# Kernel optimization log

Hardware: AMD Instinct MI355X
Metric: run time of the kernel (lower is better)

Reference implementation:

```python
import jax, jax.numpy as jnp
import numpy as np

HS = 1024
IMS = 4096
NHEAD = 16
EPS = 1e-5


def _layer_norm(x, g, b):
    mu = jnp.mean(x, axis=-1, keepdims=True)
    var = jnp.mean(jnp.square(x - mu), axis=-1, keepdims=True)
    return (x - mu) * jax.lax.rsqrt(var + EPS) * g + b


def setup_inputs() -> dict:
    key = jax.random.key(0)
    ks = jax.random.split(key, 10)
    B, S = 16, 512
    x = jax.random.normal(ks[0], (B, S, HS), dtype=jnp.float32)
    input_mask = jnp.zeros((B, S), dtype=jnp.float32)  # additive mask, 0 = attend
    sc = 0.02
    return {
        "x": x,
        "input_mask": input_mask,
        "qkv_w": jax.random.normal(ks[1], (3 * HS, HS), jnp.float32) * sc,
        "qkv_b": jnp.zeros((3 * HS,), jnp.float32),
        "attn_ow": jax.random.normal(ks[2], (HS, HS), jnp.float32) * sc,
        "attn_ob": jnp.zeros((HS,), jnp.float32),
        "ln1_g": jnp.ones((HS,), jnp.float32),
        "ln1_b": jnp.zeros((HS,), jnp.float32),
        "inter_w": jax.random.normal(ks[3], (IMS, HS), jnp.float32) * sc,
        "inter_b": jnp.zeros((IMS,), jnp.float32),
        "out_w": jax.random.normal(ks[4], (HS, IMS), jnp.float32) * sc,
        "out_b": jnp.zeros((HS,), jnp.float32),
        "ln2_g": jnp.ones((HS,), jnp.float32),
        "ln2_b": jnp.zeros((HS,), jnp.float32),
    }


def reference(x, input_mask, qkv_w, qkv_b, attn_ow, attn_ob, ln1_g, ln1_b,
              inter_w, inter_b, out_w, out_b, ln2_g, ln2_b):
    B, S, H = x.shape
    d = H // NHEAD
    # ---- self-attention block (pre_layer_norm=True, eval mode => no dropout) ----
    resid = x
    y = _layer_norm(x, ln1_g, ln1_b)
    qkv = jnp.einsum('bsh,eh->bse', y, qkv_w) + qkv_b  # [B,S,3H]
    q, k, v = jnp.split(qkv, 3, axis=-1)
    q = q.reshape(B, S, NHEAD, d)
    k = k.reshape(B, S, NHEAD, d)
    v = v.reshape(B, S, NHEAD, d)
    scores = jnp.einsum('bqnd,bknd->bnqk', q, k) / jnp.sqrt(jnp.float32(d))
    scores = scores + input_mask[:, None, None, :]  # additive padding mask
    probs = jax.nn.softmax(scores, axis=-1)
    ctx = jnp.einsum('bnqk,bknd->bqnd', probs, v).reshape(B, S, H)
    attn_out = jnp.einsum('bsh,oh->bso', ctx, attn_ow) + attn_ob
    x = resid + attn_out
    # ---- FFN block ----
    resid = x
    y = _layer_norm(x, ln2_g, ln2_b)
    h = jax.nn.relu(jnp.einsum('bsh,ih->bsi', y, inter_w) + inter_b)
    ffn_out = jnp.einsum('bsi,oi->bso', h, out_w) + out_b
    return resid + ffn_out
```

## Files before the change

### kernel.cpp

```cpp
#include <hip/hip_runtime.h>


using f32x4  = __attribute__((ext_vector_type(4))) float;
using f32x16 = __attribute__((ext_vector_type(16))) float;
using s16x8  = __attribute__((ext_vector_type(8))) short;
using i32x4  = __attribute__((ext_vector_type(4))) int;

__device__ __forceinline__ unsigned short f2bf(float f) {
    unsigned x = __builtin_bit_cast(unsigned, f);
    return (unsigned short)((x + 0x7fffu + ((x >> 16) & 1u)) >> 16);
}

#define GLL16(gptr, lptr)                                                     \
    __builtin_amdgcn_global_load_lds(                                         \
        (const __attribute__((address_space(1))) void*)(gptr),                \
        (__attribute__((address_space(3))) void*)(lptr), 16, 0, 0)

__global__ __launch_bounds__(256) void wconv_kernel(
    const float* __restrict__ w0, const float* __restrict__ w1,
    const float* __restrict__ w2, const float* __restrict__ w3,
    unsigned short* __restrict__ o0, unsigned short* __restrict__ o1,
    unsigned short* __restrict__ o2, unsigned short* __restrict__ o3) {
    long idx = (long)blockIdx.x * 256 + threadIdx.x;
    const float* src;
    unsigned short* dst;
    long rel;
    if (idx < 786432L)        { src = w0; dst = o0; rel = idx; }
    else if (idx < 1048576L)  { src = w1; dst = o1; rel = idx - 786432L; }
    else if (idx < 2097152L)  { src = w2; dst = o2; rel = idx - 1048576L; }
    else                      { src = w3; dst = o3; rel = idx - 2097152L; }
    float4 v = *(const float4*)(src + rel * 4);
    ushort4 o;
    o.x = f2bf(v.x); o.y = f2bf(v.y); o.z = f2bf(v.z); o.w = f2bf(v.w);
    *(ushort4*)(dst + rel * 4) = o;
}

__global__ __launch_bounds__(256) void ln_kernel(
    const float* __restrict__ x, const float* __restrict__ gw,
    const float* __restrict__ bw, unsigned short* __restrict__ y) {
    __shared__ float rbuf[8];
    const int row = blockIdx.x;
    const int t = threadIdx.x;
    const float* xr = x + (size_t)row * 1024;
    float4 v = *(const float4*)(xr + t * 4);
    float s  = v.x + v.y + v.z + v.w;
    float ss = v.x * v.x + v.y * v.y + v.z * v.z + v.w * v.w;
#pragma unroll
    for (int sh = 1; sh < 64; sh <<= 1) {
        s  += __shfl_xor(s, sh, 64);
        ss += __shfl_xor(ss, sh, 64);
    }
    int w = t >> 6;
    if ((t & 63) == 0) { rbuf[w * 2] = s; rbuf[w * 2 + 1] = ss; }
    __syncthreads();
    s  = rbuf[0] + rbuf[2] + rbuf[4] + rbuf[6];
    ss = rbuf[1] + rbuf[3] + rbuf[5] + rbuf[7];
    float mu  = s * (1.f / 1024.f);
    float var = ss * (1.f / 1024.f) - mu * mu;
    float rs  = rsqrtf(var + 1e-5f);
    float4 gv = *(const float4*)(gw + t * 4);
    float4 bv = *(const float4*)(bw + t * 4);
    ushort4 o;
    o.x = f2bf((v.x - mu) * rs * gv.x + bv.x);
    o.y = f2bf((v.y - mu) * rs * gv.y + bv.y);
    o.z = f2bf((v.z - mu) * rs * gv.z + bv.z);
    o.w = f2bf((v.w - mu) * rs * gv.w + bv.w);
    *(ushort4*)(y + (size_t)row * 1024 + t * 4) = o;
}

template <bool RELU, bool RESID, bool OUT_BF16>
__global__ __launch_bounds__(256, 2) void gemm_bt(
    const unsigned short* __restrict__ A, const unsigned short* __restrict__ Bw,
    const float* __restrict__ bias, const float* __restrict__ resid,
    void* __restrict__ Cout, int M, int N, int K) {
    __shared__ char smem[2 * 128 * 64 * 2];
    char* As = smem;
    char* Bs = smem + 128 * 64 * 2;

    const int tid = threadIdx.x;
    const int lane = tid & 63;
    const int w = tid >> 6;
    const int wr = w >> 1, wc = w & 1;
    const int g = lane >> 4;
    const int fr = lane & 15;
    const int m0 = blockIdx.y * 128;
    const int n0 = blockIdx.x * 128;

    f32x4 acc[4][4] = {};

    for (int kt = 0; kt < K; kt += 64) {
#pragma unroll
        for (int c = 0; c < 4; ++c) {
            int lin = (c * 256 + tid) * 16;
            int row = lin >> 7;
            int Lb = lin ^ ((row & 7) << 4);
            int colb = Lb & 127;
            const char* ga = (const char*)A + ((size_t)(m0 + row) * K + kt) * 2 + colb;
            const char* gb = (const char*)Bw + ((size_t)(n0 + row) * K + kt) * 2 + colb;
            GLL16(ga, As + lin);
            GLL16(gb, Bs + lin);
        }
        __syncthreads();
#pragma unroll
        for (int ks = 0; ks < 2; ++ks) {
            s16x8 af[4], bf[4];
#pragma unroll
            for (int mi = 0; mi < 4; ++mi) {
                int row = wr * 64 + mi * 16 + fr;
                int off = (row << 7) + ((ks * 64 + g * 16) ^ ((row & 7) << 4));
                af[mi] = *(const s16x8*)(As + off);
            }
#pragma unroll
            for (int ni = 0; ni < 4; ++ni) {
                int row = wc * 64 + ni * 16 + fr;
                int off = (row << 7) + ((ks * 64 + g * 16) ^ ((row & 7) << 4));
                bf[ni] = *(const s16x8*)(Bs + off);
            }
#pragma unroll
            for (int mi = 0; mi < 4; ++mi)
#pragma unroll
                for (int ni = 0; ni < 4; ++ni)
                    acc[mi][ni] = __builtin_amdgcn_mfma_f32_16x16x32_bf16(
                        af[mi], bf[ni], acc[mi][ni], 0, 0, 0);
        }
        __syncthreads();
    }

    float bv[4];
#pragma unroll
    for (int ni = 0; ni < 4; ++ni) bv[ni] = bias[n0 + wc * 64 + ni * 16 + fr];
#pragma unroll
    for (int mi = 0; mi < 4; ++mi) {
#pragma unroll
        for (int r = 0; r < 4; ++r) {
            int row = m0 + wr * 64 + mi * 16 + g * 4 + r;
#pragma unroll
            for (int ni = 0; ni < 4; ++ni) {
                int col = n0 + wc * 64 + ni * 16 + fr;
                float v = acc[mi][ni][r] + bv[ni];
                if (RELU) v = v > 0.f ? v : 0.f;
                if (RESID) v += resid[(size_t)row * N + col];
                if (OUT_BF16)
                    ((unsigned short*)Cout)[(size_t)row * N + col] = f2bf(v);
                else
                    ((float*)Cout)[(size_t)row * N + col] = v;
            }
        }
    }
}

__global__ __launch_bounds__(512, 2) void attn_kernel(
    const unsigned short* __restrict__ qkv, const float* __restrict__ mask,
    unsigned short* __restrict__ ctx) {
    extern __shared__ char smem[];

    const int tid = threadIdx.x;
    const int lane = tid & 63;
    const int w = tid >> 6;
    const int l31 = lane & 31;
    const int hi = lane >> 5;
    const int bh = blockIdx.x >> 1;
    const int b = bh >> 4, h = bh & 15;
    const int qt = (blockIdx.x & 1) * 256 + w * 32;

    const size_t rstr = 3072;
    const unsigned short* qbase = qkv + (size_t)b * 512 * rstr + h * 64;
    const unsigned short* kbase = qbase + 1024;
    const unsigned short* vbase = qbase + 2048;
    const float* mrow = mask + b * 512;

    s16x8 qf[4];
#pragma unroll
    for (int kc = 0; kc < 4; ++kc)
        qf[kc] = *(const s16x8*)(qbase + (size_t)(qt + l31) * rstr + kc * 16 + hi * 8);

    f32x16 O0 = {}, O1 = {};
    float m = -3e38f, l = 0.f;
    const int bpbase = 36 * hi * 4;

    auto stage = [&](int kt, int bufsel) {
        char* Kb = smem + bufsel * 16384;
        char* Vb = smem + 32768 + bufsel * 16384;
#pragma unroll
        for (int c = 0; c < 2; ++c) {
            int lin = (c * 512 + tid) * 16;
            int row = lin >> 7;
            int colb = (lin & 127) ^ ((row & 7) << 4);
            GLL16((const char*)kbase + (size_t)(kt * 128 + row) * rstr * 2 + colb,
                  Kb + lin);
        }
        int s = tid & 127, dg = tid >> 7;
        const unsigned short* vsrc = vbase + (size_t)(kt * 128 + s) * rstr + dg * 16;
        union { i32x4 v; unsigned short u[8]; } v0, v1;
        v0.v = *(const i32x4*)vsrc;
        v1.v = *(const i32x4*)(vsrc + 8);
#pragma unroll
        for (int j = 0; j < 8; ++j) {
            int d = dg * 16 + j;
            *(unsigned short*)(Vb + d * 256 + ((s * 2) ^ ((d & 15) << 4))) = v0.u[j];
        }
#pragma unroll
        for (int j = 0; j < 8; ++j) {
            int d = dg * 16 + 8 + j;
            *(unsigned short*)(Vb + d * 256 + ((s * 2) ^ ((d & 15) << 4))) = v1.u[j];
        }
    };

    const float C   = 0.18033688f;
    const float L2E = 1.44269504f;

    stage(0, 0);
    __syncthreads();

    for (int kt = 0; kt < 4; ++kt) {
        const int cur = kt & 1;
        if (kt < 3) stage(kt + 1, cur ^ 1);
        char* Kb = smem + cur * 16384;
        char* Vb = smem + 32768 + cur * 16384;
        const int swzk = (l31 & 7) << 4;

        f32x16 sc[4];
#pragma unroll
        for (int t = 0; t < 4; ++t) {
            f32x16 a = {};
#pragma unroll
            for (int kc = 0; kc < 4; ++kc) {
                s16x8 kf = *(const s16x8*)(Kb + (32 * t + l31) * 128 +
                                           ((kc * 32 + hi * 16) ^ swzk));
                a = __builtin_amdgcn_mfma_f32_32x32x16_bf16(kf, qf[kc], a, 0, 0, 0);
            }
            sc[t] = a;
        }

        float tm = -3e38f;
#pragma unroll
        for (int t = 0; t < 4; ++t) {
#pragma unroll
            for (int k2 = 0; k2 < 4; ++k2) {
                f32x4 mk = *(const f32x4*)(mrow + kt * 128 + 32 * t + 8 * k2 + 4 * hi);
#pragma unroll
                for (int i = 0; i < 4; ++i) {
                    float v = sc[t][4 * k2 + i] * C + mk[i] * L2E;
                    sc[t][4 * k2 + i] = v;
                    tm = fmaxf(tm, v);
                }
            }
        }
        tm = fmaxf(tm, __shfl_xor(tm, 32, 64));

        if (__any(tm > m + 11.0f)) {
            float mn = fmaxf(m, tm);
            float fac = exp2f(m - mn);
            m = mn;
            l *= fac;
            int fi = __float_as_int(fac);
#pragma unroll
            for (int r = 0; r < 16; ++r) {
                int q2 = (r & 3) + 8 * (r >> 2);
                float fq = __int_as_float(
                    __builtin_amdgcn_ds_bpermute(bpbase + q2 * 4, fi));
                O0[r] *= fq;
                O1[r] *= fq;
            }
        }

        float ts = 0.f;
#pragma unroll
        for (int t = 0; t < 4; ++t)
#pragma unroll
            for (int r = 0; r < 16; ++r) {
                float p = exp2f(sc[t][r] - m);
                sc[t][r] = p;
                ts += p;
            }
        ts += __shfl_xor(ts, 32, 64);
        l += ts;

        unsigned pk01[4][4], pk23[4][4];
#pragma unroll
        for (int t = 0; t < 4; ++t)
#pragma unroll
            for (int k = 0; k < 4; ++k) {
                unsigned r0, r1;
                asm("v_cvt_pk_bf16_f32 %0, %1, %2"
                    : "=v"(r0) : "v"(sc[t][4 * k]), "v"(sc[t][4 * k + 1]));
                asm("v_cvt_pk_bf16_f32 %0, %1, %2"
                    : "=v"(r1) : "v"(sc[t][4 * k + 2]), "v"(sc[t][4 * k + 3]));
                pk01[t][k] = r0;
                pk23[t][k] = r1;
            }

#pragma unroll
        for (int t = 0; t < 4; ++t)
#pragma unroll
            for (int cc = 0; cc < 2; ++cc) {
                unsigned a0 = pk01[t][2 * cc], b0 = pk01[t][2 * cc + 1];
                unsigned c0 = pk23[t][2 * cc], d0 = pk23[t][2 * cc + 1];
                asm("v_permlane32_swap_b32 %0, %1" : "+v"(a0), "+v"(b0));
                asm("v_permlane32_swap_b32 %0, %1" : "+v"(c0), "+v"(d0));
                union { unsigned u[4]; s16x8 v; } pf;
                pf.u[0] = a0;
                pf.u[1] = c0;
                pf.u[2] = b0;
                pf.u[3] = d0;
                const int kc = 2 * t + cc;
                {
                    int row = l31;
                    s16x8 vf = *(const s16x8*)(Vb + row * 256 +
                               ((kc * 32 + hi * 16) ^ ((row & 15) << 4)));
                    O0 = __builtin_amdgcn_mfma_f32_32x32x16_bf16(pf.v, vf, O0, 0, 0, 0);
                }
                {
                    int row = 32 + l31;
                    s16x8 vf = *(const s16x8*)(Vb + row * 256 +
                               ((kc * 32 + hi * 16) ^ ((row & 15) << 4)));
                    O1 = __builtin_amdgcn_mfma_f32_32x32x16_bf16(pf.v, vf, O1, 0, 0, 0);
                }
            }
        __syncthreads();
    }

    const int li = __float_as_int(l);
#pragma unroll
    for (int r = 0; r < 16; ++r) {
        int q2 = (r & 3) + 8 * (r >> 2);
        float lq = __int_as_float(__builtin_amdgcn_ds_bpermute(bpbase + q2 * 4, li));
        float inv = 1.f / lq;
        size_t rowg = (size_t)(b * 512 + qt + q2 + 4 * hi) * 1024 + h * 64;
        ctx[rowg + l31]      = f2bf(O0[r] * inv);
        ctx[rowg + 32 + l31] = f2bf(O1[r] * inv);
    }
}

extern "C" void kernel_launch(void* const* d_in, const int* in_sizes, int n_in,
                              void* d_out, int out_size, void* d_ws, size_t ws_size,
                              hipStream_t stream) {
    const float* x    = (const float*)d_in[0];
    const float* mask = (const float*)d_in[1];
    const float* qkvw = (const float*)d_in[2];
    const float* qkvb = (const float*)d_in[3];
    const float* ow   = (const float*)d_in[4];
    const float* ob   = (const float*)d_in[5];
    const float* ln1g = (const float*)d_in[6];
    const float* ln1b = (const float*)d_in[7];
    const float* iw   = (const float*)d_in[8];
    const float* ib   = (const float*)d_in[9];
    const float* o2w  = (const float*)d_in[10];
    const float* o2b  = (const float*)d_in[11];
    const float* ln2g = (const float*)d_in[12];
    const float* ln2b = (const float*)d_in[13];

    char* ws = (char*)d_ws;
    unsigned short* qkvbuf = (unsigned short*)(ws);
    unsigned short* ybuf   = (unsigned short*)(ws + 50331648);
    unsigned short* cbuf   = (unsigned short*)(ws + 67108864);
    float*          x2     = (float*)(ws + 83886080);
    unsigned short* wq     = (unsigned short*)(ws + 117440512);
    unsigned short* wo     = (unsigned short*)(ws + 123731968);
    unsigned short* wi     = (unsigned short*)(ws + 125829120);
    unsigned short* wo2    = (unsigned short*)(ws + 134217728);
    unsigned short* hbuf   = (unsigned short*)(ws);

    wconv_kernel<<<12288, 256, 0, stream>>>(qkvw, ow, iw, o2w, wq, wo, wi, wo2);
    ln_kernel<<<8192, 256, 0, stream>>>(x, ln1g, ln1b, ybuf);
    gemm_bt<false, false, true><<<dim3(24, 64), 256, 0, stream>>>(
        ybuf, wq, qkvb, nullptr, qkvbuf, 8192, 3072, 1024);
    hipFuncSetAttribute(reinterpret_cast<const void*>(attn_kernel),
                        hipFuncAttributeMaxDynamicSharedMemorySize, 65536);
    attn_kernel<<<512, 512, 65536, stream>>>(qkvbuf, mask, cbuf);
    gemm_bt<false, true, false><<<dim3(8, 64), 256, 0, stream>>>(
        cbuf, wo, ob, x, x2, 8192, 1024, 1024);
    ln_kernel<<<8192, 256, 0, stream>>>(x2, ln2g, ln2b, cbuf);
    gemm_bt<true, false, true><<<dim3(32, 64), 256, 0, stream>>>(
        cbuf, wi, ib, nullptr, hbuf, 8192, 4096, 1024);
    gemm_bt<false, true, false><<<dim3(8, 64), 256, 0, stream>>>(
        hbuf, wo2, o2b, x2, (float*)d_out, 8192, 1024, 4096);
}
```

Baseline: 307.6 us.

## Add double-buffered 256x256 GEMM kernel and XCD-aware block swizzle

Adds a new 512-thread GEMM with 256x256 tiles, double-buffered LDS staging through global_load_lds and interleaved prefetch of the next K tile in four phases with setprio around the MFMAs. It is used for the QKV and FFN-intermediate GEMMs. A workgroup-ID swizzle that groups blocks by L&7, likely aimed at the chiplet layout, is added to both GEMM kernels. The goal is more data reuse per tile and hidden load latency, in exchange for 128KB of LDS per block, lower occupancy and fewer blocks on wide grids.

```diff
diff --git a/kernel.cpp b/kernel.cpp
--- a/kernel.cpp
+++ b/kernel.cpp
@@ -83,8 +83,11 @@
     const int wr = w >> 1, wc = w & 1;
     const int g = lane >> 4;
     const int fr = lane & 15;
-    const int m0 = blockIdx.y * 128;
-    const int n0 = blockIdx.x * 128;
+    const int nwg = gridDim.x * gridDim.y;
+    const int L = blockIdx.y * gridDim.x + blockIdx.x;
+    const int swz = (L & 7) * (nwg >> 3) + (L >> 3);
+    const int m0 = (swz / gridDim.x) * 128;
+    const int n0 = (swz % gridDim.x) * 128;
 
     f32x4 acc[4][4] = {};
 
@@ -147,6 +150,129 @@
             }
         }
     }
+}
+
+template <bool RELU, bool OUT_BF16>
+__global__ __launch_bounds__(512, 2) void gemm256(
+    const unsigned short* __restrict__ A, const unsigned short* __restrict__ Bw,
+    const float* __restrict__ bias, void* __restrict__ Cout,
+    int M, int N, int K) {
+    extern __shared__ char lds[];
+
+    const int tid = threadIdx.x;
+    const int lane = tid & 63;
+    const int w = tid >> 6;
+    const int wm = w >> 2, wn = w & 3;
+    const int g = lane >> 4, fr = lane & 15;
+
+    const int nwg = gridDim.x * gridDim.y;
+    const int L = blockIdx.y * gridDim.x + blockIdx.x;
+    const int swz = (L & 7) * (nwg >> 3) + (L >> 3);
+    const int m0 = (swz / gridDim.x) * 256;
+    const int n0 = (swz % gridDim.x) * 256;
+
+    const int NT = K >> 6;
+
+    auto stageA = [&](int t, int h) {
+        char* dst = lds + (t & 1) * 32768 + h * 16384;
+#pragma unroll
+        for (int c2 = 0; c2 < 2; ++c2) {
+            int lin = (c2 * 512 + tid) * 16;
+            int row = lin >> 7;
+            int colb = (lin & 127) ^ ((row & 7) << 4);
+            GLL16((const char*)A + ((size_t)(m0 + h * 128 + row) * K + t * 64) * 2 + colb,
+                  dst + lin);
+        }
+    };
+    auto stageB = [&](int t, int h) {
+        char* dst = lds + 65536 + (t & 1) * 32768 + h * 16384;
+#pragma unroll
+        for (int c2 = 0; c2 < 2; ++c2) {
+            int lin = (c2 * 512 + tid) * 16;
+            int row = lin >> 7;
+            int colb = (lin & 127) ^ ((row & 7) << 4);
+            GLL16((const char*)Bw + ((size_t)(n0 + h * 128 + row) * K + t * 64) * 2 + colb,
+                  dst + lin);
+        }
+    };
+
+    f32x4 acc[2][4][2][2] = {};
+    s16x8 af[4][2];
+    s16x8 bf[2][2];
+
+    stageA(0, 0); stageB(0, 0); stageB(0, 1); stageA(0, 1);
+    asm volatile("s_waitcnt vmcnt(4)" ::: "memory");
+    __builtin_amdgcn_s_barrier();
+
+    for (int t = 0; t < NT; ++t) {
+        char* Ab = lds + (t & 1) * 32768;
+        char* Bb = lds + 65536 + (t & 1) * 32768;
+        const bool more = (t + 1 < NT);
+#pragma unroll
+        for (int p = 0; p < 4; ++p) {
+            const int ha = p >> 1, hb = p & 1;
+            if (more) {
+                if (p == 0)      stageA(t + 1, 0);
+                else if (p == 1) stageB(t + 1, 0);
+                else if (p == 2) stageB(t + 1, 1);
+                else             stageA(t + 1, 1);
+            }
+            if ((p & 1) == 0) {
+#pragma unroll
+                for (int mi2 = 0; mi2 < 4; ++mi2) {
+                    int row = ha * 128 + wm * 64 + mi2 * 16 + fr;
+#pragma unroll
+                    for (int ks = 0; ks < 2; ++ks)
+                        af[mi2][ks] = *(const s16x8*)(Ab + (row << 7) +
+                                       ((ks * 64 + g * 16) ^ ((row & 7) << 4)));
+                }
+            }
+#pragma unroll
+            for (int ni2 = 0; ni2 < 2; ++ni2) {
+                int row = hb * 128 + wn * 32 + ni2 * 16 + fr;
+#pragma unroll
+                for (int ks = 0; ks < 2; ++ks)
+                    bf[ni2][ks] = *(const s16x8*)(Bb + (row << 7) +
+                                   ((ks * 64 + g * 16) ^ ((row & 7) << 4)));
+            }
+            asm volatile("s_waitcnt vmcnt(4)" ::: "memory");
+            __builtin_amdgcn_s_barrier();
+            asm volatile("s_waitcnt lgkmcnt(0)" ::: "memory");
+            __builtin_amdgcn_sched_barrier(0);
+            __builtin_amdgcn_s_setprio(1);
+#pragma unroll
+            for (int mi2 = 0; mi2 < 4; ++mi2)
+#pragma unroll
+                for (int ni2 = 0; ni2 < 2; ++ni2)
+#pragma unroll
+                    for (int ks = 0; ks < 2; ++ks)
+                        acc[ha][mi2][hb][ni2] = __builtin_amdgcn_mfma_f32_16x16x32_bf16(
+                            af[mi2][ks], bf[ni2][ks], acc[ha][mi2][hb][ni2], 0, 0, 0);
+            __builtin_amdgcn_s_setprio(0);
+            __builtin_amdgcn_s_barrier();
+        }
+    }
+
+#pragma unroll
+    for (int ha = 0; ha < 2; ++ha)
+#pragma unroll
+        for (int mi2 = 0; mi2 < 4; ++mi2)
+#pragma unroll
+            for (int r = 0; r < 4; ++r) {
+                int row = m0 + ha * 128 + wm * 64 + mi2 * 16 + g * 4 + r;
+#pragma unroll
+                for (int hb = 0; hb < 2; ++hb)
+#pragma unroll
+                    for (int ni2 = 0; ni2 < 2; ++ni2) {
+                        int col = n0 + hb * 128 + wn * 32 + ni2 * 16 + fr;
+                        float v = acc[ha][mi2][hb][ni2][r] + bias[col];
+                        if (RELU) v = v > 0.f ? v : 0.f;
+                        if (OUT_BF16)
+                            ((unsigned short*)Cout)[(size_t)row * N + col] = f2bf(v);
+                        else
+                            ((float*)Cout)[(size_t)row * N + col] = v;
+                    }
+            }
 }
 
 __global__ __launch_bounds__(512, 2) void attn_kernel(
@@ -361,18 +487,23 @@
     unsigned short* wo2    = (unsigned short*)(ws + 134217728);
     unsigned short* hbuf   = (unsigned short*)(ws);
 
+    hipFuncSetAttribute(reinterpret_cast<const void*>(attn_kernel),
+                        hipFuncAttributeMaxDynamicSharedMemorySize, 65536);
+    hipFuncSetAttribute(reinterpret_cast<const void*>(&gemm256<false, true>),
+                        hipFuncAttributeMaxDynamicSharedMemorySize, 131072);
+    hipFuncSetAttribute(reinterpret_cast<const void*>(&gemm256<true, true>),
+                        hipFuncAttributeMaxDynamicSharedMemorySize, 131072);
+
     wconv_kernel<<<12288, 256, 0, stream>>>(qkvw, ow, iw, o2w, wq, wo, wi, wo2);
     ln_kernel<<<8192, 256, 0, stream>>>(x, ln1g, ln1b, ybuf);
-    gemm_bt<false, false, true><<<dim3(24, 64), 256, 0, stream>>>(
-        ybuf, wq, qkvb, nullptr, qkvbuf, 8192, 3072, 1024);
-    hipFuncSetAttribute(reinterpret_cast<const void*>(attn_kernel),
-                        hipFuncAttributeMaxDynamicSharedMemorySize, 65536);
+    gemm256<false, true><<<dim3(12, 32), 512, 131072, stream>>>(
+        ybuf, wq, qkvb, qkvbuf, 8192, 3072, 1024);
     attn_kernel<<<512, 512, 65536, stream>>>(qkvbuf, mask, cbuf);
     gemm_bt<false, true, false><<<dim3(8, 64), 256, 0, stream>>>(
         cbuf, wo, ob, x, x2, 8192, 1024, 1024);
     ln_kernel<<<8192, 256, 0, stream>>>(x2, ln2g, ln2b, cbuf);
-    gemm_bt<true, false, true><<<dim3(32, 64), 256, 0, stream>>>(
-        cbuf, wi, ib, nullptr, hbuf, 8192, 4096, 1024);
+    gemm256<true, true><<<dim3(16, 32), 512, 131072, stream>>>(
+        cbuf, wi, ib, hbuf, 8192, 4096, 1024);
     gemm_bt<false, true, false><<<dim3(8, 64), 256, 0, stream>>>(
         hbuf, wo2, o2b, x2, (float*)d_out, 8192, 1024, 4096);
 }
```

New measurement: 312.4 us. Within noise of the previous version (+1.6%).

## Replace GEMM with triple-buffered 128x256 tile kernel with prefetch and XCD swizzle

Applied to the files above, without the earlier changes.

The GEMM kernel is rewritten to use 512 threads per block and 128x256 output tiles. LDS becomes three dynamic buffers filled with global_load_lds, so the tile two K-steps ahead is prefetched while the current one is computed. Each iteration waits on vmcnt and uses raw s_barrier instead of two full __syncthreads. Block indices are swizzled across the 8 XCDs, and s_setprio raises wave priority during the MFMA phase. Using 144KB of LDS per block limits occupancy to one block per CU, and the wider N tile halves the grid, so overlap has to make up for fewer resident waves.

```diff
diff --git a/kernel.cpp b/kernel.cpp
--- a/kernel.cpp
+++ b/kernel.cpp
@@ -15,6 +15,8 @@
     __builtin_amdgcn_global_load_lds(                                         \
         (const __attribute__((address_space(1))) void*)(gptr),                \
         (__attribute__((address_space(3))) void*)(lptr), 16, 0, 0)
+
+#define VMC(N) asm volatile("s_waitcnt vmcnt(" #N ")" ::: "memory")
 
 __global__ __launch_bounds__(256) void wconv_kernel(
     const float* __restrict__ w0, const float* __restrict__ w1,
@@ -69,74 +71,102 @@
 }
 
 template <bool RELU, bool RESID, bool OUT_BF16>
-__global__ __launch_bounds__(256, 2) void gemm_bt(
+__global__ __launch_bounds__(512, 2) void gemm_dp(
     const unsigned short* __restrict__ A, const unsigned short* __restrict__ Bw,
     const float* __restrict__ bias, const float* __restrict__ resid,
     void* __restrict__ Cout, int M, int N, int K) {
-    __shared__ char smem[2 * 128 * 64 * 2];
-    char* As = smem;
-    char* Bs = smem + 128 * 64 * 2;
+    extern __shared__ char lds[];
 
     const int tid = threadIdx.x;
     const int lane = tid & 63;
     const int w = tid >> 6;
-    const int wr = w >> 1, wc = w & 1;
-    const int g = lane >> 4;
-    const int fr = lane & 15;
-    const int m0 = blockIdx.y * 128;
-    const int n0 = blockIdx.x * 128;
+    const int wm = w >> 2, wn = w & 3;
+    const int g = lane >> 4, fr = lane & 15;
+
+    const int nwg = gridDim.x * gridDim.y;
+    const int L = blockIdx.y * gridDim.x + blockIdx.x;
+    const int swz = (L & 7) * (nwg >> 3) + (L >> 3);
+    const int m0 = (swz / gridDim.x) * 128;
+    const int n0 = (swz % gridDim.x) * 256;
+
+    const int NT = K >> 6;
+
+    auto stage = [&](int t) {
+        char* dst = lds + (t % 3) * 49152;
+#pragma unroll
+        for (int c = 0; c < 2; ++c) {
+            int lin = (c * 512 + tid) * 16;
+            int row = lin >> 7;
+            int colb = (lin & 127) ^ ((row & 7) << 4);
+            GLL16((const char*)A + ((size_t)(m0 + row) * K + t * 64) * 2 + colb,
+                  dst + lin);
+        }
+#pragma unroll
+        for (int c = 0; c < 4; ++c) {
+            int lin = (c * 512 + tid) * 16;
+            int row = lin >> 7;
+            int colb = (lin & 127) ^ ((row & 7) << 4);
+            GLL16((const char*)Bw + ((size_t)(n0 + row) * K + t * 64) * 2 + colb,
+                  dst + 16384 + lin);
+        }
+    };
 
     f32x4 acc[4][4] = {};
 
-    for (int kt = 0; kt < K; kt += 64) {
-#pragma unroll
-        for (int c = 0; c < 4; ++c) {
-            int lin = (c * 256 + tid) * 16;
-            int row = lin >> 7;
-            int Lb = lin ^ ((row & 7) << 4);
-            int colb = Lb & 127;
-            const char* ga = (const char*)A + ((size_t)(m0 + row) * K + kt) * 2 + colb;
-            const char* gb = (const char*)Bw + ((size_t)(n0 + row) * K + kt) * 2 + colb;
-            GLL16(ga, As + lin);
-            GLL16(gb, Bs + lin);
-        }
-        __syncthreads();
-#pragma unroll
-        for (int ks = 0; ks < 2; ++ks) {
-            s16x8 af[4], bf[4];
-#pragma unroll
-            for (int mi = 0; mi < 4; ++mi) {
-                int row = wr * 64 + mi * 16 + fr;
-                int off = (row << 7) + ((ks * 64 + g * 16) ^ ((row & 7) << 4));
-                af[mi] = *(const s16x8*)(As + off);
-            }
+    stage(0);
+    stage(1);
+    VMC(6);
+    __builtin_amdgcn_s_barrier();
+
+    for (int t = 0; t < NT; ++t) {
+        char* Ab = lds + (t % 3) * 49152;
+        char* Bb = Ab + 16384;
+        s16x8 af[4][2], bf[4][2];
+#pragma unroll
+        for (int mi = 0; mi < 4; ++mi) {
+            int row = wm * 64 + mi * 16 + fr;
+#pragma unroll
+            for (int ks = 0; ks < 2; ++ks)
+                af[mi][ks] = *(const s16x8*)(Ab + (row << 7) +
+                              ((ks * 64 + g * 16) ^ ((row & 7) << 4)));
+        }
+#pragma unroll
+        for (int ni = 0; ni < 4; ++ni) {
+            int row = wn * 64 + ni * 16 + fr;
+#pragma unroll
+            for (int ks = 0; ks < 2; ++ks)
+                bf[ni][ks] = *(const s16x8*)(Bb + (row << 7) +
+                              ((ks * 64 + g * 16) ^ ((row & 7) << 4)));
+        }
+        if (t + 2 < NT) { stage(t + 2); VMC(6); }
+        else if (t + 1 < NT) { VMC(0); }
+        __builtin_amdgcn_s_barrier();
+        asm volatile("s_waitcnt lgkmcnt(0)" ::: "memory");
+        __builtin_amdgcn_sched_barrier(0);
+        __builtin_amdgcn_s_setprio(1);
+#pragma unroll
+        for (int mi = 0; mi < 4; ++mi)
+#pragma unroll
+            for (int ni = 0; ni < 4; ++ni)
+#pragma unroll
+                for (int ks = 0; ks < 2; ++ks)
+                    acc[mi][ni] = __builtin_amdgcn_mfma_f32_16x16x32_bf16(
+                        af[mi][ks], bf[ni][ks], acc[mi][ni], 0, 0, 0);
+        __builtin_amdgcn_s_setprio(0);
+        __builtin_amdgcn_s_barrier();
+    }
+
+    float bv[4];
+#pragma unroll
+    for (int ni = 0; ni < 4; ++ni) bv[ni] = bias[n0 + wn * 64 + ni * 16 + fr];
+#pragma unroll
+    for (int mi = 0; mi < 4; ++mi) {
+#pragma unroll
+        for (int r = 0; r < 4; ++r) {
+            int row = m0 + wm * 64 + mi * 16 + g * 4 + r;
 #pragma unroll
             for (int ni = 0; ni < 4; ++ni) {
-                int row = wc * 64 + ni * 16 + fr;
-                int off = (row << 7) + ((ks * 64 + g * 16) ^ ((row & 7) << 4));
-                bf[ni] = *(const s16x8*)(Bs + off);
-            }
-#pragma unroll
-            for (int mi = 0; mi < 4; ++mi)
-#pragma unroll
-                for (int ni = 0; ni < 4; ++ni)
-                    acc[mi][ni] = __builtin_amdgcn_mfma_f32_16x16x32_bf16(
-                        af[mi], bf[ni], acc[mi][ni], 0, 0, 0);
-        }
-        __syncthreads();
-    }
-
-    float bv[4];
-#pragma unroll
-    for (int ni = 0; ni < 4; ++ni) bv[ni] = bias[n0 + wc * 64 + ni * 16 + fr];
-#pragma unroll
-    for (int mi = 0; mi < 4; ++mi) {
-#pragma unroll
-        for (int r = 0; r < 4; ++r) {
-            int row = m0 + wr * 64 + mi * 16 + g * 4 + r;
-#pragma unroll
-            for (int ni = 0; ni < 4; ++ni) {
-                int col = n0 + wc * 64 + ni * 16 + fr;
+                int col = n0 + wn * 64 + ni * 16 + fr;
                 float v = acc[mi][ni][r] + bv[ni];
                 if (RELU) v = v > 0.f ? v : 0.f;
                 if (RESID) v += resid[(size_t)row * N + col];
@@ -361,18 +391,25 @@
     unsigned short* wo2    = (unsigned short*)(ws + 134217728);
     unsigned short* hbuf   = (unsigned short*)(ws);
 
+    hipFuncSetAttribute(reinterpret_cast<const void*>(attn_kernel),
+                        hipFuncAttributeMaxDynamicSharedMemorySize, 65536);
+    hipFuncSetAttribute(reinterpret_cast<const void*>(&gemm_dp<false, false, true>),
+                        hipFuncAttributeMaxDynamicSharedMemorySize, 147456);
+    hipFuncSetAttribute(reinterpret_cast<const void*>(&gemm_dp<false, true, false>),
+                        hipFuncAttributeMaxDynamicSharedMemorySize, 147456);
+    hipFuncSetAttribute(reinterpret_cast<const void*>(&gemm_dp<true, false, true>),
+                        hipFuncAttributeMaxDynamicSharedMemorySize, 147456);
+
     wconv_kernel<<<12288, 256, 0, stream>>>(qkvw, ow, iw, o2w, wq, wo, wi, wo2);
     ln_kernel<<<8192, 256, 0, stream>>>(x, ln1g, ln1b, ybuf);
-    gemm_bt<false, false, true><<<dim3(24, 64), 256, 0, stream>>>(
+    gemm_dp<false, false, true><<<dim3(12, 64), 512, 147456, stream>>>(
         ybuf, wq, qkvb, nullptr, qkvbuf, 8192, 3072, 1024);
-    hipFuncSetAttribute(reinterpret_cast<const void*>(attn_kernel),
-                        hipFuncAttributeMaxDynamicSharedMemorySize, 65536);
     attn_kernel<<<512, 512, 65536, stream>>>(qkvbuf, mask, cbuf);
-    gemm_bt<false, true, false><<<dim3(8, 64), 256, 0, stream>>>(
+    gemm_dp<false, true, false><<<dim3(4, 64), 512, 147456, stream>>>(
         cbuf, wo, ob, x, x2, 8192, 1024, 1024);
     ln_kernel<<<8192, 256, 0, stream>>>(x2, ln2g, ln2b, cbuf);
-    gemm_bt<true, false, true><<<dim3(32, 64), 256, 0, stream>>>(
+    gemm_dp<true, false, true><<<dim3(16, 64), 512, 147456, stream>>>(
         cbuf, wi, ib, nullptr, hbuf, 8192, 4096, 1024);
-    gemm_bt<false, true, false><<<dim3(8, 64), 256, 0, stream>>>(
+    gemm_dp<false, true, false><<<dim3(4, 64), 512, 147456, stream>>>(
         hbuf, wo2, o2b, x2, (float*)d_out, 8192, 1024, 4096);
 }
```

Result: slower. 322.6 us (+4.9%).
